# Optimization experiments

Hardware: AMD Instinct MI355X
Metric: run time of the kernel (lower is better)

Reference implementation:

```python
import jax, jax.numpy as jnp
import numpy as np

B, N, M, T, D, NH = 64, 1024, 32, 8, 512, 8
OUT = 1000
NSO, NSA = N // 4, N // 8
DH = D // NH


def _conv(x, w, b):
    y = jax.lax.conv_general_dilated(x, w, (1, 1), 'SAME', dimension_numbers=('NCHW', 'OIHW', 'NCHW'))
    return y + b[None, :, None, None]


def _bn(x, g, b):
    # BatchNorm2d in train mode: per-batch statistics over (B, H, W)
    m = x.mean(axis=(0, 2, 3), keepdims=True)
    v = x.var(axis=(0, 2, 3), keepdims=True)
    return (x - m) * jax.lax.rsqrt(v + 1e-5) * g[None, :, None, None] + b[None, :, None, None]


def _mp2(x):
    b_, c, h, w = x.shape
    return x.reshape(b_, c, h // 2, 2, w // 2, 2).max(axis=(3, 5))


def _ln(x, g, b):
    m = x.mean(-1, keepdims=True)
    v = x.var(-1, keepdims=True)
    return (x - m) * jax.lax.rsqrt(v + 1e-5) * g + b


def _glu(x):
    a, b = jnp.split(x, 2, axis=-1)
    return a * jax.nn.sigmoid(b)


def setup_inputs():
    ks = iter(jax.random.split(jax.random.key(0), 64))

    def nrm(shape, fan_in):
        return jax.random.normal(next(ks), shape, jnp.float32) / np.float32(np.sqrt(fan_in))

    inp = {}
    inp['x'] = jax.random.normal(next(ks), (B, 3, 64, 64), jnp.float32)
    inp['c1w'] = nrm((16, 3, 3, 3), 27); inp['c1b'] = jnp.zeros((16,))
    inp['bn1g'] = jnp.ones((16,)); inp['bn1b'] = jnp.zeros((16,))
    inp['c2w'] = nrm((32, 16, 3, 3), 144); inp['c2b'] = jnp.zeros((32,))
    inp['bn2g'] = jnp.ones((32,)); inp['bn2b'] = jnp.zeros((32,))
    inp['c3w'] = nrm((64, 32, 3, 3), 288); inp['c3b'] = jnp.zeros((64,))
    inp['bn3g'] = jnp.ones((64,)); inp['bn3b'] = jnp.zeros((64,))
    inp['c4w'] = nrm((64, 64, 3, 3), 576); inp['c4b'] = jnp.zeros((64,))
    inp['bn4g'] = jnp.ones((64,)); inp['bn4b'] = jnp.zeros((64,))
    inp['fc1w'] = nrm((256, 256), 256); inp['fc1b'] = jnp.zeros((256,))
    inp['fc2w'] = nrm((128, D), 128); inp['fc2b'] = jnp.zeros((D,))
    inp['kvw'] = nrm((D, D), D); inp['kvb'] = jnp.zeros((D,))
    inp['kvlg'] = jnp.ones((D,)); inp['kvlb'] = jnp.zeros((D,))
    inp['synw'] = nrm((D + N, 2 * N), D + N); inp['synb'] = jnp.zeros((2 * N,))
    inp['synlg'] = jnp.ones((N,)); inp['synlb'] = jnp.zeros((N,))
    inp['nlm_w1'] = nrm((N, M, 256), M); inp['nlm_b1'] = jnp.zeros((N, 256))
    inp['nlm_w2'] = nrm((N, 128), 128); inp['nlm_b2'] = jnp.zeros((N,))
    inp['start_act'] = nrm((N,), N)
    inp['start_trace'] = nrm((N, M), N + M)
    inp['dec_a'] = jax.random.uniform(next(ks), (NSA,), jnp.float32, 0.0, 3.0)
    inp['dec_o'] = jax.random.uniform(next(ks), (NSO,), jnp.float32, 0.0, 3.0)
    inp['qw'] = nrm((NSA, D), NSA); inp['qb'] = jnp.zeros((D,))
    inp['attn_inw'] = nrm((D, 3 * D), D); inp['attn_inb'] = jnp.zeros((3 * D,))
    inp['attn_ow'] = nrm((D, D), D); inp['attn_ob'] = jnp.zeros((D,))
    inp['op_w1'] = nrm((NSO, 256), NSO); inp['op_b1'] = jnp.zeros((256,))
    inp['op_l1g'] = jnp.ones((256,)); inp['op_l1b'] = jnp.zeros((256,))
    inp['op_w2'] = nrm((256, 64), 256); inp['op_b2'] = jnp.zeros((64,))
    inp['op_l2g'] = jnp.ones((64,)); inp['op_l2b'] = jnp.zeros((64,))
    inp['op_w3'] = nrm((64, OUT), 64); inp['op_b3'] = jnp.zeros((OUT,))
    inp['aL'] = jax.random.randint(next(ks), (NSA,), 0, N)
    inp['aR'] = jax.random.randint(next(ks), (NSA,), 0, N)
    inp['oL'] = jax.random.randint(next(ks), (NSO,), 0, N)
    inp['oR'] = jax.random.randint(next(ks), (NSO,), 0, N)
    inp['task_idx'] = 0
    return inp


def _forward(x, c1w, c1b, bn1g, bn1b, c2w, c2b, bn2g, bn2b, c3w, c3b, bn3g, bn3b, c4w, c4b, bn4g, bn4b, fc1w, fc1b, fc2w, fc2b, kvw, kvb, kvlg, kvlb, synw, synb, synlg, synlb, nlm_w1, nlm_b1, nlm_w2, nlm_b2, start_act, start_trace, dec_a, dec_o, qw, qb, attn_inw, attn_inb, attn_ow, attn_ob, op_w1, op_b1, op_l1g, op_l1b, op_w2, op_b2, op_l2g, op_l2b, op_w3, op_b3, aL, aR, oL, oR):
    # --- AdaptiveCNNEncoder (3-channel branch) ---
    h = jax.nn.relu(_bn(_conv(x, c1w, c1b), bn1g, bn1b))
    h = jax.nn.relu(_bn(_conv(h, c2w, c2b), bn2g, bn2b))
    h = _mp2(h)
    h = jax.nn.relu(_bn(_conv(h, c3w, c3b), bn3g, bn3b))
    h = _mp2(h)
    h = jax.nn.relu(_bn(_conv(h, c4w, c4b), bn4g, bn4b))
    b_, c, hh, ww = h.shape
    # AdaptiveAvgPool2d((2,2)): mean over equal blocks (16x16 -> 2x2)
    h = h.reshape(b_, c, 2, hh // 2, 2, ww // 2).mean(axis=(3, 5)).reshape(b_, c * 4)
    enc = _glu(h @ fc1w + fc1b) @ fc2w + fc2b            # (B, D)
    kv = _ln(enc @ kvw + kvb, kvlg, kvlb)                # single kv token

    Wq, Wk, Wv = jnp.split(attn_inw, 3, axis=1)
    bq, bk, bv = jnp.split(attn_inb, 3)
    kh = (kv @ Wk + bk).reshape(B, NH, DH)
    vh = (kv @ Wv + bv).reshape(B, NH, DH)

    r_a = jnp.exp(-jnp.clip(dec_a, 0.0, 15.0))           # (NSA,)
    r_o = jnp.exp(-jnp.clip(dec_o, 0.0, 15.0))           # (NSO,)

    act0 = jnp.broadcast_to(start_act, (B, N))
    trace0 = jnp.broadcast_to(start_trace, (B, N, M))
    ao0 = act0[:, oL] * act0[:, oR]                      # initial out-sync accumulators
    bo0 = jnp.ones_like(ao0)
    inv_log_out = np.float32(1.0 / np.log(OUT))
    inv_sqrt_dh = np.float32(1.0 / np.sqrt(DH))

    def tick(carry, t):
        act, trace, aa, ba, ao, bo = carry
        pp = act[:, aL] * act[:, aR]
        first = (t == 0)
        aa = jnp.where(first, pp, r_a * aa + pp)
        ba = jnp.where(first, jnp.ones_like(ba), r_a * ba + 1.0)
        sync_a = aa * jax.lax.rsqrt(ba + 1e-8)
        qv = sync_a @ qw + qb
        qh = (qv @ Wq + bq).reshape(B, NH, DH)
        logits = jnp.einsum('bhd,bhd->bh', qh, kh) * inv_sqrt_dh
        w = jax.nn.softmax(logits[..., None], axis=-1)[..., 0]  # single key -> ones
        attn_out = (w[..., None] * vh).reshape(B, D) @ attn_ow + attn_ob
        pre = jnp.concatenate([attn_out, act], axis=-1)
        state = _ln(_glu(pre @ synw + synb), synlg, synlb)
        trace = jnp.concatenate([trace[:, :, 1:], state[:, :, None]], axis=-1)
        # per-neuron private MLPs, batched: (B,N,M)x(N,M,256) -> GLU -> (N,128) -> scalar
        hid = _glu(jnp.einsum('bnm,nmh->bnh', trace, nlm_w1) + nlm_b1)
        act = jnp.einsum('bnh,nh->bn', hid, nlm_w2) + nlm_b2
        po = act[:, oL] * act[:, oR]
        ao = r_o * ao + po
        bo = r_o * bo + 1.0
        sync_o = ao * jax.lax.rsqrt(bo + 1e-8)
        h1 = jax.nn.relu(_ln(sync_o @ op_w1 + op_b1, op_l1g, op_l1b))
        h2 = jax.nn.relu(_ln(h1 @ op_w2 + op_b2, op_l2g, op_l2b))
        pred = h2 @ op_w3 + op_b3
        p = jax.nn.softmax(pred, axis=-1)
        ent = -jnp.sum(p * jnp.log(p + 1e-10), axis=-1)
        ne = ent * inv_log_out
        cert = jnp.stack([ne, 1.0 - ne], axis=-1)
        return (act, trace, aa, ba, ao, bo), (pred, cert)

    carry0 = (act0, trace0, jnp.zeros((B, NSA), jnp.float32), jnp.zeros((B, NSA), jnp.float32), ao0, bo0)
    _, (preds, certs) = jax.lax.scan(tick, carry0, jnp.arange(T))
    return jnp.transpose(preds, (1, 2, 0)), jnp.transpose(certs, (1, 2, 0))


def reference(x, c1w, c1b, bn1g, bn1b, c2w, c2b, bn2g, bn2b, c3w, c3b, bn3g, bn3b, c4w, c4b, bn4g, bn4b, fc1w, fc1b, fc2w, fc2b, kvw, kvb, kvlg, kvlb, synw, synb, synlg, synlb, nlm_w1, nlm_b1, nlm_w2, nlm_b2, start_act, start_trace, dec_a, dec_o, qw, qb, attn_inw, attn_inb, attn_ow, attn_ob, op_w1, op_b1, op_l1g, op_l1b, op_w2, op_b2, op_l2g, op_l2b, op_w3, op_b3, aL, aR, oL, oR, task_idx):
    del task_idx  # single task; all task-indexed params are for task 0
    return _forward(x, c1w, c1b, bn1g, bn1b, c2w, c2b, bn2g, bn2b, c3w, c3b, bn3g, bn3b, c4w, c4b, bn4g, bn4b, fc1w, fc1b, fc2w, fc2b, kvw, kvb, kvlg, kvlb, synw, synb, synlg, synlb, nlm_w1, nlm_b1, nlm_w2, nlm_b2, start_act, start_trace, dec_a, dec_o, qw, qb, attn_inw, attn_inb, attn_ow, attn_ob, op_w1, op_b1, op_l1g, op_l1b, op_w2, op_b2, op_l2g, op_l2b, op_w3, op_b3, aL, aR, oL, oR)
```

## Files before the change

kernel.cpp:

```cpp
#include <hip/hip_runtime.h>
#include <math.h>

constexpr int B_ = 64, N_ = 1024, M_ = 32, T_ = 8;
constexpr int OUT_ = 1000, NSO_ = 256;

#define DEVFN __device__ __forceinline__

typedef __attribute__((ext_vector_type(8))) short bf16x8;
typedef __attribute__((ext_vector_type(4))) float f32x4;

DEVFN float blockReduceSum(float v, float* buf) {
  int t = threadIdx.x;
  buf[t] = v; __syncthreads();
  for (int off = blockDim.x >> 1; off > 0; off >>= 1) {
    if (t < off) buf[t] += buf[t + off];
    __syncthreads();
  }
  float r = buf[0];
  __syncthreads();
  return r;
}

DEVFN float sigmoidf_(float x) { return 1.f / (1.f + __expf(-x)); }

DEVFN unsigned short f2bf(float f) {
  unsigned u = __float_as_uint(f);
  unsigned r = (u + 0x7FFFu + ((u >> 16) & 1u)) >> 16;
  return (unsigned short)r;
}
DEVFN float bf2f(unsigned short h) { return __uint_as_float((unsigned)h << 16); }

template<int NW>
DEVFN float bsum(float v, float* red) {
  #pragma unroll
  for (int o = 32; o > 0; o >>= 1) v += __shfl_xor(v, o);
  int w = threadIdx.x >> 6, ln = threadIdx.x & 63;
  if (ln == 0) red[w] = v;
  __syncthreads();
  if (w == 0) {
    float x = (ln < NW) ? red[ln] : 0.f;
    #pragma unroll
    for (int o = 8; o > 0; o >>= 1) x += __shfl_xor(x, o);
    if (ln == 0) red[0] = x;
  }
  __syncthreads();
  float r = red[0];
  __syncthreads();
  return r;
}

template<int NW>
DEVFN float bmax(float v, float* red) {
  #pragma unroll
  for (int o = 32; o > 0; o >>= 1) v = fmaxf(v, __shfl_xor(v, o));
  int w = threadIdx.x >> 6, ln = threadIdx.x & 63;
  if (ln == 0) red[w] = v;
  __syncthreads();
  if (w == 0) {
    float x = (ln < NW) ? red[ln] : -INFINITY;
    #pragma unroll
    for (int o = 8; o > 0; o >>= 1) x = fmaxf(x, __shfl_xor(x, o));
    if (ln == 0) red[0] = x;
  }
  __syncthreads();
  float r = red[0];
  __syncthreads();
  return r;
}

__global__ __launch_bounds__(256)
void k_w1t(const float* __restrict__ w1, unsigned short* __restrict__ w1t) {
  int n = blockIdx.x;
  __shared__ float tile[32][260];
  const float* src = w1 + (size_t)n * 8192;
  for (int i = threadIdx.x; i < 8192; i += 256)
    tile[i >> 8][i & 255] = src[i];
  __syncthreads();
  int c = threadIdx.x;
  unsigned short* dst = w1t + ((size_t)n * 256 + c) * 32;
  #pragma unroll
  for (int q = 0; q < 8; ++q) {
    ushort4 o;
    o.x = f2bf(tile[q * 4 + 0][c]); o.y = f2bf(tile[q * 4 + 1][c]);
    o.z = f2bf(tile[q * 4 + 2][c]); o.w = f2bf(tile[q * 4 + 3][c]);
    *reinterpret_cast<ushort4*>(dst + q * 4) = o;
  }
}

__global__ __launch_bounds__(256)
void k_synwt(const float* __restrict__ synw2, unsigned short* __restrict__ Bt) {
  int j0 = blockIdx.x * 64, k0 = blockIdx.y * 64;
  __shared__ float tile[64][65];
  for (int i = threadIdx.x; i < 4096; i += 256) {
    int kk = i >> 6, jj = i & 63;
    tile[kk][jj] = synw2[(size_t)(k0 + kk) * 2048 + j0 + jj];
  }
  __syncthreads();
  int jj = threadIdx.x >> 2, kq = (threadIdx.x & 3) * 16;
  unsigned short* dst = Bt + (size_t)(j0 + jj) * 1024 + k0 + kq;
  #pragma unroll
  for (int q = 0; q < 4; ++q) {
    ushort4 o;
    o.x = f2bf(tile[kq + q * 4 + 0][jj]); o.y = f2bf(tile[kq + q * 4 + 1][jj]);
    o.z = f2bf(tile[kq + q * 4 + 2][jj]); o.w = f2bf(tile[kq + q * 4 + 3][jj]);
    *reinterpret_cast<ushort4*>(dst + q * 4) = o;
  }
}

template<int CIN, int COUT, int HW, int TY, int XV, int CICH, int MODE, int KSPLIT, int COSPLIT>
__global__ __launch_bounds__(256)
void k_conv_tiled(const float* __restrict__ in, const float* __restrict__ wgl,
                  const float2* __restrict__ ssin, float* __restrict__ outp) {
  constexpr int XQ = HW / XV;
  constexpr int NCG = 4;
  constexpr int CPT = COUT / (NCG * COSPLIT);
  constexpr int PADW = HW + 8;
  constexpr int NROW = TY + 2;
  constexpr int CINB = CIN / KSPLIT;
  constexpr int NCH = CINB / CICH;
  static_assert(XQ * TY == 64, "spatial threads per co-group must be 64");
  __shared__ __align__(16) float ins[CICH][NROW][PADW];

  const int b   = blockIdx.x;
  const int y0  = blockIdx.y * TY;
  const int cs  = (COSPLIT > 1) ? (int)(blockIdx.z % COSPLIT) : 0;
  const int ks  = (KSPLIT > 1) ? (int)(blockIdx.z / COSPLIT) : 0;
  const int co0 = cs * (COUT / COSPLIT);
  const int tid = threadIdx.x;
  const int sp  = tid & 63;
  const int cg  = __builtin_amdgcn_readfirstlane(tid >> 6);
  const int xq  = sp % XQ;
  const int yr  = sp / XQ;
  const int x0  = xq * XV;

  float acc[CPT][XV];
  #pragma unroll
  for (int j = 0; j < CPT; ++j)
    #pragma unroll
    for (int k = 0; k < XV; ++k) acc[j][k] = 0.f;

  for (int ch = 0; ch < NCH; ++ch) {
    const int ci0 = ks * CINB + ch * CICH;
    __syncthreads();
    constexpr int NEL = CICH * NROW * PADW;
    for (int i = tid; i < NEL; i += 256) {
      int col = i % PADW;
      int row = (i / PADW) % NROW;
      int ci  = i / (PADW * NROW);
      int gx = col - 4;
      int gy = y0 + row - 1;
      float v = 0.f;
      if (gx >= 0 && gx < HW && gy >= 0 && gy < HW) {
        if (MODE == 0) {
          v = in[((size_t)(b * CIN + ci0 + ci) * HW + gy) * HW + gx];
        } else if (MODE == 1) {
          float2 s = ssin[ci0 + ci];
          v = fmaxf(fmaf(in[((size_t)(b * CIN + ci0 + ci) * HW + gy) * HW + gx], s.x, s.y), 0.f);
        } else {
          float2 s = ssin[ci0 + ci];
          const float* p = in + ((size_t)(b * CIN + ci0 + ci) * (2 * HW) + 2 * gy) * (2 * HW) + 2 * gx;
          float v0 = fmaf(p[0],          s.x, s.y);
          float v1 = fmaf(p[1],          s.x, s.y);
          float v2 = fmaf(p[2 * HW],     s.x, s.y);
          float v3 = fmaf(p[2 * HW + 1], s.x, s.y);
          v = fmaxf(fmaxf(fmaxf(v0, v1), fmaxf(v2, v3)), 0.f);
        }
      }
      ins[ci][row][col] = v;
    }
    __syncthreads();

    for (int ci = 0; ci < CICH; ++ci) {
      const float* wci = wgl + ((size_t)(co0 + cg * CPT) * CIN + (ci0 + ci)) * 9;
      #pragma unroll
      for (int dy = 0; dy < 3; ++dy) {
        const float* r = &ins[ci][yr + dy][x0 + 4];
        float win[XV + 2];
        win[0] = r[-1];
        if constexpr (XV == 4) {
          float4 m = *reinterpret_cast<const float4*>(r);
          win[1] = m.x; win[2] = m.y; win[3] = m.z; win[4] = m.w;
        } else if constexpr (XV == 2) {
          float2 m = *reinterpret_cast<const float2*>(r);
          win[1] = m.x; win[2] = m.y;
        } else {
          win[1] = r[0];
        }
        win[XV + 1] = r[XV];
        #pragma unroll
        for (int j = 0; j < CPT; ++j) {
          const float* wj = wci + (size_t)j * CIN * 9 + dy * 3;
          float w0 = wj[0], w1 = wj[1], w2 = wj[2];
          #pragma unroll
          for (int k = 0; k < XV; ++k)
            acc[j][k] = fmaf(win[k], w0, fmaf(win[k + 1], w1, fmaf(win[k + 2], w2, acc[j][k])));
        }
      }
    }
  }

  const size_t pofs = (size_t)ks * B_ * COUT * HW * HW;
  #pragma unroll
  for (int j = 0; j < CPT; ++j) {
    float* op = outp + pofs + (((size_t)b * COUT + co0 + cg * CPT + j) * HW + y0 + yr) * HW + x0;
    if constexpr (XV == 4)
      *reinterpret_cast<float4*>(op) = make_float4(acc[j][0], acc[j][1], acc[j][2], acc[j][3]);
    else if constexpr (XV == 2)
      *reinterpret_cast<float2*>(op) = make_float2(acc[j][0], acc[j][1]);
    else
      *op = acc[j][0];
  }
}

template<int C, int HW2, int NS>
__global__ __launch_bounds__(256)
void k_bn_stats(const float* __restrict__ x, float* __restrict__ part) {
  int c = blockIdx.x, s = blockIdx.y, ns = gridDim.y;
  const int Npc = B_ * HW2;
  constexpr size_t PSTR = (size_t)B_ * C * HW2;
  float s1 = 0.f, s2 = 0.f;
  for (int ii = s * 256 + threadIdx.x; ii < Npc; ii += ns * 256) {
    int b = ii / HW2, pos = ii % HW2;
    size_t base = ((size_t)b * C + c) * HW2 + pos;
    float v = x[base];
    #pragma unroll
    for (int q = 1; q < NS; ++q) v += x[base + q * PSTR];
    s1 += v; s2 += v * v;
  }
  __shared__ float r1[256], r2[256];
  r1[threadIdx.x] = s1; r2[threadIdx.x] = s2; __syncthreads();
  for (int off = 128; off > 0; off >>= 1) {
    if (threadIdx.x < off) { r1[threadIdx.x] += r1[threadIdx.x + off]; r2[threadIdx.x] += r2[threadIdx.x + off]; }
    __syncthreads();
  }
  if (threadIdx.x == 0) {
    part[(c * ns + s) * 2 + 0] = r1[0];
    part[(c * ns + s) * 2 + 1] = r2[0];
  }
}

__global__ void k_bn_finalize(const float* __restrict__ part, int C, int ns, float inv_n,
                              const float* __restrict__ g, const float* __restrict__ bb,
                              float2* __restrict__ ss) {
  int c = threadIdx.x;
  if (c >= C) return;
  float s1 = 0.f, s2 = 0.f;
  for (int s = 0; s < ns; ++s) { s1 += part[(c * ns + s) * 2]; s2 += part[(c * ns + s) * 2 + 1]; }
  float m = s1 * inv_n;
  float var = s2 * inv_n - m * m;
  float rstd = rsqrtf(var + 1e-5f);
  float sc = g[c] * rstd;
  ss[c] = make_float2(sc, bb[c] - m * sc);
}

__global__ __launch_bounds__(256)
void k_avgpool_bn(const float* __restrict__ x, const float2* __restrict__ ss,
                  float* __restrict__ outp) {
  constexpr size_t PSTR = (size_t)B_ * 64 * 256;
  int idx = blockIdx.x * 256 + threadIdx.x;
  if (idx >= B_ * 256) return;
  int b = idx >> 8;
  int r = idx & 255;
  int c = r >> 2, i = (r >> 1) & 1, j = r & 1;
  float2 s = ss[c];
  const float* p = x + ((size_t)(b * 64 + c) * 16 + i * 8) * 16 + j * 8;
  float sum = 0.f;
  #pragma unroll
  for (int yy = 0; yy < 8; ++yy)
    #pragma unroll
    for (int xx = 0; xx < 8; ++xx) {
      size_t o = yy * 16 + xx;
      float v = p[o] + p[o + PSTR] + p[o + 2 * PSTR] + p[o + 3 * PSTR];
      sum += fmaxf(fmaf(v, s.x, s.y), 0.f);
    }
  outp[idx] = sum * (1.f / 64.f);
}

template<int K, int NOUT>
__global__ __launch_bounds__(256)
void k_gemm_part(const float* __restrict__ A, const float* __restrict__ W, int ldw,
                 float* __restrict__ part) {
  int jt = blockIdx.x, ks = blockIdx.y;
  int k0 = ks * 64;
  __shared__ float As[64][65];
  for (int i = threadIdx.x; i < 4096; i += 256) {
    int r = i >> 6, c = i & 63;
    As[r][c] = A[(size_t)r * K + k0 + c];
  }
  __syncthreads();
  int jsub = threadIdx.x & 31;
  int bg = threadIdx.x >> 5;
  int j = jt * 32 + jsub;
  float acc[8] = {0.f, 0.f, 0.f, 0.f, 0.f, 0.f, 0.f, 0.f};
  const float* wp = W + (size_t)k0 * ldw + j;
  #pragma unroll 8
  for (int kk = 0; kk < 64; ++kk) {
    float w = wp[(size_t)kk * ldw];
    #pragma unroll
    for (int r = 0; r < 8; ++r) acc[r] = fmaf(As[bg * 8 + r][kk], w, acc[r]);
  }
  float* pp = part + (size_t)ks * 64 * NOUT + j;
  #pragma unroll
  for (int r = 0; r < 8; ++r) pp[(size_t)(bg * 8 + r) * NOUT] = acc[r];
}

__global__ __launch_bounds__(256)
void k_syn_mfma(const unsigned short* __restrict__ Abf, const unsigned short* __restrict__ Bt,
                float* __restrict__ part) {
  const int jt = blockIdx.x, ks = blockIdx.y;
  const int w = threadIdx.x >> 6, lane = threadIdx.x & 63;
  const int col = lane & 15, kg = lane >> 4;
  const int jcol = jt * 64 + w * 16 + col;
  const int k0 = ks * 256;
  f32x4 acc[4];
  #pragma unroll
  for (int mt = 0; mt < 4; ++mt) acc[mt] = (f32x4){0.f, 0.f, 0.f, 0.f};

  #pragma unroll
  for (int kb = 0; kb < 8; ++kb) {
    const int kk = k0 + kb * 32 + kg * 8;
    bf16x8 bfr = *reinterpret_cast<const bf16x8*>(Bt + (size_t)jcol * 1024 + kk);
    #pragma unroll
    for (int mt = 0; mt < 4; ++mt) {
      bf16x8 a = *reinterpret_cast<const bf16x8*>(Abf + (size_t)(mt * 16 + col) * 1024 + kk);
      acc[mt] = __builtin_amdgcn_mfma_f32_16x16x32_bf16(a, bfr, acc[mt], 0, 0, 0);
    }
  }
  #pragma unroll
  for (int mt = 0; mt < 4; ++mt) {
    int b0 = mt * 16 + kg * 4;
    #pragma unroll
    for (int r = 0; r < 4; ++r)
      part[((size_t)ks * 64 + b0 + r) * 2048 + jcol] = acc[mt][r];
  }
}

template<int NOUT, int NO_FIN, int KS, bool GLU_, bool LN_>
__global__ __launch_bounds__(256)
void k_fc_reduce(const float* __restrict__ part, const float* __restrict__ bias, int bstride,
                 const float* __restrict__ lng, const float* __restrict__ lnb,
                 float* __restrict__ outp) {
  constexpr int R = (NO_FIN + 255) / 256;
  int b = blockIdx.x, t = threadIdx.x;
  const float* bp = bias + (size_t)b * bstride;
  float v[R];
  #pragma unroll
  for (int r = 0; r < R; ++r) {
    int j = t + r * 256;
    if (j < NO_FIN) {
      float za = bp[j];
      float zb = GLU_ ? bp[j + NO_FIN] : 0.f;
      #pragma unroll
      for (int ks = 0; ks < KS; ++ks) {
        const float* pr = part + ((size_t)ks * 64 + b) * NOUT;
        za += pr[j];
        if (GLU_) zb += pr[j + NO_FIN];
      }
      v[r] = GLU_ ? za * sigmoidf_(zb) : za;
    } else v[r] = 0.f;
  }
  if (LN_) {
    __shared__ float red[256];
    float s1 = 0.f, s2 = 0.f;
    #pragma unroll
    for (int r = 0; r < R; ++r) { s1 += v[r]; s2 += v[r] * v[r]; }
    s1 = blockReduceSum(s1, red);
    s2 = blockReduceSum(s2, red);
    float mu = s1 / (float)NO_FIN;
    float rstd = rsqrtf(s2 / (float)NO_FIN - mu * mu + 1e-5f);
    #pragma unroll
    for (int r = 0; r < R; ++r) {
      int j = t + r * 256;
      if (j < NO_FIN) outp[(size_t)b * NO_FIN + j] = fmaf((v[r] - mu) * rstd, lng[j], lnb[j]);
    }
  } else {
    #pragma unroll
    for (int r = 0; r < R; ++r) {
      int j = t + r * 256;
      if (j < NO_FIN) outp[(size_t)b * NO_FIN + j] = v[r];
    }
  }
}

__global__ __launch_bounds__(1024)
void k_syn_reduce(const float* __restrict__ part, const float* __restrict__ syncst,
                  const float* __restrict__ g, const float* __restrict__ bb,
                  unsigned short* __restrict__ trace, int slot) {
  int b = blockIdx.x, t = threadIdx.x;
  __shared__ float red[16];
  float za = syncst[b * 2048 + t];
  float zb = syncst[b * 2048 + 1024 + t];
  #pragma unroll
  for (int ks = 0; ks < 4; ++ks) {
    const float* pr = part + ((size_t)ks * 64 + b) * 2048;
    za += pr[t];
    zb += pr[t + 1024];
  }
  float v = za * sigmoidf_(zb);
  float s1 = bsum<16>(v, red);
  float s2 = bsum<16>(v * v, red);
  float mu = s1 * (1.f / 1024.f);
  float rstd = rsqrtf(s2 * (1.f / 1024.f) - mu * mu + 1e-5f);
  trace[((size_t)t * 64 + b) * 32 + slot] = f2bf(fmaf((v - mu) * rstd, g[t], bb[t]));
}

__global__ __launch_bounds__(256)
void k_init(const float* __restrict__ sa, const float* __restrict__ st,
            const int* __restrict__ oL, const int* __restrict__ oR,
            float* __restrict__ act, unsigned short* __restrict__ act_bf,
            unsigned short* __restrict__ trace,
            float* __restrict__ ao, float* __restrict__ bo) {
  int idx = blockIdx.x * 256 + threadIdx.x;
  if (idx < B_ * N_ * M_) {
    int n = idx >> 11, m = idx & 31;
    trace[idx] = f2bf(st[n * 32 + m]);
  }
  if (idx < B_ * N_) {
    float v = sa[idx % N_];
    act[idx] = v;
    act_bf[idx] = f2bf(v);
  }
  if (idx < B_ * NSO_) {
    int i = idx % NSO_;
    ao[idx] = sa[oL[i]] * sa[oR[i]];
    bo[idx] = 1.f;
  }
}

__global__ __launch_bounds__(128)
void k_nlm_mfma(const unsigned short* __restrict__ trace, const unsigned short* __restrict__ w1t,
                const float* __restrict__ b1, const float* __restrict__ w2,
                const float* __restrict__ b2, float* __restrict__ act,
                unsigned short* __restrict__ act_bf, int tick) {
  const int w = threadIdx.x >> 6, lane = threadIdx.x & 63;
  const int n = blockIdx.x * 2 + w;
  const int col = lane & 15, kg = lane >> 4;
  __shared__ __align__(16) unsigned short ldsA[2][64][40];
  {
    const uint4* src = reinterpret_cast<const uint4*>(trace + ((size_t)n * 64 + lane) * 32);
    uint4 r0 = src[0], r1 = src[1], r2 = src[2], r3 = src[3];
    uint4* d = reinterpret_cast<uint4*>(&ldsA[w][lane][0]);
    d[0] = r0; d[1] = r1; d[2] = r2; d[3] = r3;
  }
  bf16x8 bf[16];
  float b1v[16], w2v[8];
  #pragma unroll
  for (int nt = 0; nt < 16; ++nt) {
    bf[nt] = *reinterpret_cast<const bf16x8*>(w1t + (((size_t)n * 256 + nt * 16 + col) * 32 + kg * 8));
    b1v[nt] = b1[n * 256 + nt * 16 + col];
  }
  #pragma unroll
  for (int nt = 0; nt < 8; ++nt) w2v[nt] = w2[n * 128 + nt * 16 + col];
  const float b2n = b2[n];
  const int kbase = kg * 8 + ((tick + 1) & 31);
  __syncthreads();
  #pragma unroll
  for (int mt = 0; mt < 4; ++mt) {
    const int brow = mt * 16 + col;
    bf16x8 af;
    #pragma unroll
    for (int j = 0; j < 8; ++j)
      af[j] = (short)ldsA[w][brow][(kbase + j) & 31];
    f32x4 acc[16];
    #pragma unroll
    for (int nt = 0; nt < 16; ++nt)
      acc[nt] = __builtin_amdgcn_mfma_f32_16x16x32_bf16(af, bf[nt], (f32x4){0.f, 0.f, 0.f, 0.f}, 0, 0, 0);
    float v0 = 0.f, v1 = 0.f, v2 = 0.f, v3 = 0.f;
    #pragma unroll
    for (int nt = 0; nt < 8; ++nt) {
      f32x4 za = acc[nt], zb = acc[nt + 8];
      float ba = b1v[nt], bg = b1v[nt + 8], wv = w2v[nt];
      v0 = fmaf((za[0] + ba) * sigmoidf_(zb[0] + bg), wv, v0);
      v1 = fmaf((za[1] + ba) * sigmoidf_(zb[1] + bg), wv, v1);
      v2 = fmaf((za[2] + ba) * sigmoidf_(zb[2] + bg), wv, v2);
      v3 = fmaf((za[3] + ba) * sigmoidf_(zb[3] + bg), wv, v3);
    }
    #pragma unroll
    for (int o = 1; o <= 8; o <<= 1) {
      v0 += __shfl_xor(v0, o); v1 += __shfl_xor(v1, o);
      v2 += __shfl_xor(v2, o); v3 += __shfl_xor(v3, o);
    }
    if (col == 0) {
      int b0 = mt * 16 + kg * 4;
      float r0 = v0 + b2n, r1 = v1 + b2n, r2 = v2 + b2n, r3 = v3 + b2n;
      act[(size_t)(b0 + 0) * 1024 + n] = r0;
      act[(size_t)(b0 + 1) * 1024 + n] = r1;
      act[(size_t)(b0 + 2) * 1024 + n] = r2;
      act[(size_t)(b0 + 3) * 1024 + n] = r3;
      act_bf[(size_t)(b0 + 0) * 1024 + n] = f2bf(r0);
      act_bf[(size_t)(b0 + 1) * 1024 + n] = f2bf(r1);
      act_bf[(size_t)(b0 + 2) * 1024 + n] = f2bf(r2);
      act_bf[(size_t)(b0 + 3) * 1024 + n] = f2bf(r3);
    }
  }
}

__global__ __launch_bounds__(1024)
void k_outpath(const float* __restrict__ act, float* __restrict__ ao, float* __restrict__ bo,
               const float* __restrict__ dec_o, const int* __restrict__ oL, const int* __restrict__ oR,
               const float* __restrict__ opw1, const float* __restrict__ opb1,
               const float* __restrict__ l1g, const float* __restrict__ l1b,
               const float* __restrict__ opw2, const float* __restrict__ opb2,
               const float* __restrict__ l2g, const float* __restrict__ l2b,
               const float* __restrict__ opw3, const float* __restrict__ opb3,
               float* __restrict__ outp, int tick) {
  int b = blockIdx.x, t = threadIdx.x;
  __shared__ float red[16];
  __shared__ float syo[256], h1s[256], h2s[64];
  __shared__ float zp1[4][256];
  __shared__ float zp2[16][64];
  const float* actb = act + (size_t)b * 1024;
  if (t < 256) {
    float po = actb[oL[t]] * actb[oR[t]];
    float r = __expf(-fminf(fmaxf(dec_o[t], 0.f), 15.f));
    int ai = b * 256 + t;
    float av = fmaf(r, ao[ai], po);
    float bv = fmaf(r, bo[ai], 1.f);
    ao[ai] = av; bo[ai] = bv;
    syo[t] = av * rsqrtf(bv + 1e-8f);
  }
  __syncthreads();
  {
    int j = t & 255, ks = t >> 8;
    float z = 0.f;
    const float* wcol = opw1 + j;
    #pragma unroll 8
    for (int k = ks * 64; k < ks * 64 + 64; ++k) z = fmaf(syo[k], wcol[k * 256], z);
    zp1[ks][j] = z;
  }
  __syncthreads();
  float h1v = 0.f;
  if (t < 256) h1v = zp1[0][t] + zp1[1][t] + zp1[2][t] + zp1[3][t] + opb1[t];
  float s1 = bsum<16>(t < 256 ? h1v : 0.f, red);
  float s2 = bsum<16>(t < 256 ? h1v * h1v : 0.f, red);
  if (t < 256) {
    float mu = s1 * (1.f / 256.f);
    float rstd = rsqrtf(s2 * (1.f / 256.f) - mu * mu + 1e-5f);
    h1s[t] = fmaxf(fmaf((h1v - mu) * rstd, l1g[t], l1b[t]), 0.f);
  }
  __syncthreads();
  {
    int j = t & 63, ks = t >> 6;
    float z = 0.f;
    const float* wcol = opw2 + j;
    #pragma unroll
    for (int k = ks * 16; k < ks * 16 + 16; ++k) z = fmaf(h1s[k], wcol[k * 64], z);
    zp2[ks][j] = z;
  }
  __syncthreads();
  if (t < 64) {
    float z2 = opb2[t];
    #pragma unroll
    for (int ks = 0; ks < 16; ++ks) z2 += zp2[ks][t];
    float a1 = z2, a2 = z2 * z2;
    #pragma unroll
    for (int o = 32; o > 0; o >>= 1) { a1 += __shfl_xor(a1, o); a2 += __shfl_xor(a2, o); }
    float mu2 = a1 * (1.f / 64.f);
    float rs2 = rsqrtf(a2 * (1.f / 64.f) - mu2 * mu2 + 1e-5f);
    h2s[t] = fmaxf(fmaf((z2 - mu2) * rs2, l2g[t], l2b[t]), 0.f);
  }
  __syncthreads();
  float z3 = 0.f;
  if (t < OUT_) {
    z3 = opb3[t];
    const float* wcol = opw3 + t;
    #pragma unroll 8
    for (int k = 0; k < 64; ++k) z3 = fmaf(h2s[k], wcol[k * OUT_], z3);
    outp[(size_t)b * (OUT_ * T_) + (size_t)t * T_ + tick] = z3;
  }
  float mx = bmax<16>(t < OUT_ ? z3 : -INFINITY, red);
  float e = (t < OUT_) ? __expf(z3 - mx) : 0.f;
  float S = bsum<16>(e, red);
  float inv = 1.f / S;
  float ep = 0.f;
  if (t < OUT_) {
    float p = e * inv;
    ep = p * __logf(p + 1e-10f);
  }
  float ent = -bsum<16>(ep, red);
  if (t == 0) {
    float ne = ent * (1.f / logf(1000.f));
    outp[(size_t)B_ * OUT_ * T_ + (size_t)b * 2 * T_ + tick]      = ne;
    outp[(size_t)B_ * OUT_ * T_ + (size_t)b * 2 * T_ + T_ + tick] = 1.f - ne;
  }
}

extern "C" void kernel_launch(void* const* d_in, const int* in_sizes, int n_in,
                              void* d_out, int out_size, void* d_ws, size_t ws_size,
                              hipStream_t stream) {
  (void)in_sizes; (void)n_in; (void)out_size; (void)ws_size;
  const float* x      = (const float*)d_in[0];
  const float* c1w    = (const float*)d_in[1];
  const float* bn1g   = (const float*)d_in[3];
  const float* bn1b   = (const float*)d_in[4];
  const float* c2w    = (const float*)d_in[5];
  const float* bn2g   = (const float*)d_in[7];
  const float* bn2b   = (const float*)d_in[8];
  const float* c3w    = (const float*)d_in[9];
  const float* bn3g   = (const float*)d_in[11];
  const float* bn3b   = (const float*)d_in[12];
  const float* c4w    = (const float*)d_in[13];
  const float* bn4g   = (const float*)d_in[15];
  const float* bn4b   = (const float*)d_in[16];
  const float* fc1w   = (const float*)d_in[17];
  const float* fc1b   = (const float*)d_in[18];
  const float* fc2w   = (const float*)d_in[19];
  const float* fc2b   = (const float*)d_in[20];
  const float* kvw    = (const float*)d_in[21];
  const float* kvb    = (const float*)d_in[22];
  const float* kvlg   = (const float*)d_in[23];
  const float* kvlb   = (const float*)d_in[24];
  const float* synw   = (const float*)d_in[25];
  const float* synb   = (const float*)d_in[26];
  const float* synlg  = (const float*)d_in[27];
  const float* synlb  = (const float*)d_in[28];
  const float* nlmw1  = (const float*)d_in[29];
  const float* nlmb1  = (const float*)d_in[30];
  const float* nlmw2  = (const float*)d_in[31];
  const float* nlmb2  = (const float*)d_in[32];
  const float* sact   = (const float*)d_in[33];
  const float* strc   = (const float*)d_in[34];
  const float* dec_o  = (const float*)d_in[36];
  const float* attn_inw = (const float*)d_in[39];
  const float* attn_inb = (const float*)d_in[40];
  const float* attn_ow  = (const float*)d_in[41];
  const float* attn_ob  = (const float*)d_in[42];
  const float* opw1   = (const float*)d_in[43];
  const float* opb1   = (const float*)d_in[44];
  const float* opl1g  = (const float*)d_in[45];
  const float* opl1b  = (const float*)d_in[46];
  const float* opw2   = (const float*)d_in[47];
  const float* opb2   = (const float*)d_in[48];
  const float* opl2g  = (const float*)d_in[49];
  const float* opl2b  = (const float*)d_in[50];
  const float* opw3   = (const float*)d_in[51];
  const float* opb3   = (const float*)d_in[52];
  const int*   oL     = (const int*)d_in[55];
  const int*   oR     = (const int*)d_in[56];
  float* outp = (float*)d_out;
  float* ws   = (float*)d_ws;

  float* c2raw = ws;
  float* c4part= ws;
  float* c1raw = ws + 8388608;
  float* c3raw = ws + 8388608;
  float* part  = ws + 4194304;
  unsigned short* trace_bf = (unsigned short*)(ws + 6291456);
  float* act   = ws + 8388608;
  float* syncst= ws + 8454144;
  float* pooled= ws + 8585216;
  float* ench  = ws + 8601600;
  float* enc   = ws + 8609792;
  float* kvbuf = ws + 8642560;
  float* vhbuf = ws + 8675328;
  float* aout  = ws + 8708096;
  float* ao    = ws + 8740864;
  float* bo    = ws + 8757248;
  unsigned short* w1t_bf   = (unsigned short*)(ws + 8777728);
  unsigned short* synw2t_bf= (unsigned short*)(ws + 12972032);
  float* bnpart= ws + 14020608;
  float2* bnss = (float2*)(ws + 14024704);
  unsigned short* act_bf = (unsigned short*)(ws + 14028800);

  k_conv_tiled<3,16,64,4,4,3,0,1,1><<<dim3(64,16),256,0,stream>>>(x, c1w, nullptr, c1raw);
  k_bn_stats<16,4096,1><<<dim3(16,32),256,0,stream>>>(c1raw, bnpart);
  k_bn_finalize<<<1,64,0,stream>>>(bnpart, 16, 32, 1.f/(float)(B_*4096), bn1g, bn1b, bnss);

  k_conv_tiled<16,32,64,2,2,16,1,1,1><<<dim3(64,32),256,0,stream>>>(c1raw, c2w, bnss, c2raw);
  k_bn_stats<32,4096,1><<<dim3(32,32),256,0,stream>>>(c2raw, bnpart);
  k_bn_finalize<<<1,64,0,stream>>>(bnpart, 32, 32, 1.f/(float)(B_*4096), bn2g, bn2b, bnss);

  k_conv_tiled<32,64,32,4,2,16,2,1,2><<<dim3(64,8,2),256,0,stream>>>(c2raw, c3w, bnss, c3raw);
  k_bn_stats<64,1024,1><<<dim3(64,16),256,0,stream>>>(c3raw, bnpart);
  k_bn_finalize<<<1,64,0,stream>>>(bnpart, 64, 16, 1.f/(float)(B_*1024), bn3g, bn3b, bnss);

  k_conv_tiled<64,64,16,4,1,16,2,4,1><<<dim3(64,4,4),256,0,stream>>>(c3raw, c4w, bnss, c4part);

  k_w1t<<<1024,256,0,stream>>>(nlmw1, w1t_bf);
  k_synwt<<<dim3(32,16),256,0,stream>>>(synw + (size_t)512 * 2048, synw2t_bf);

  k_bn_stats<64,256,4><<<dim3(64,8),256,0,stream>>>(c4part, bnpart);
  k_bn_finalize<<<1,64,0,stream>>>(bnpart, 64, 8, 1.f/(float)(B_*256), bn4g, bn4b, bnss);
  k_avgpool_bn<<<64,256,0,stream>>>(c4part, bnss, pooled);

  k_gemm_part<256,256><<<dim3(8,4),256,0,stream>>>(pooled, fc1w, 256, part);
  k_fc_reduce<256,128,4,true,false><<<64,256,0,stream>>>(part, fc1b, 0, nullptr, nullptr, ench);
  k_gemm_part<128,512><<<dim3(16,2),256,0,stream>>>(ench, fc2w, 512, part);
  k_fc_reduce<512,512,2,false,false><<<64,256,0,stream>>>(part, fc2b, 0, nullptr, nullptr, enc);
  k_gemm_part<512,512><<<dim3(16,8),256,0,stream>>>(enc, kvw, 512, part);
  k_fc_reduce<512,512,8,false,true><<<64,256,0,stream>>>(part, kvb, 0, kvlg, kvlb, kvbuf);
  k_gemm_part<512,512><<<dim3(16,8),256,0,stream>>>(kvbuf, attn_inw + 1024, 1536, part);
  k_fc_reduce<512,512,8,false,false><<<64,256,0,stream>>>(part, attn_inb + 1024, 0, nullptr, nullptr, vhbuf);
  k_gemm_part<512,512><<<dim3(16,8),256,0,stream>>>(vhbuf, attn_ow, 512, part);
  k_fc_reduce<512,512,8,false,false><<<64,256,0,stream>>>(part, attn_ob, 0, nullptr, nullptr, aout);
  k_gemm_part<512,2048><<<dim3(64,8),256,0,stream>>>(aout, synw, 2048, part);
  k_fc_reduce<2048,2048,8,false,false><<<64,256,0,stream>>>(part, synb, 0, nullptr, nullptr, syncst);

  k_init<<<8192,256,0,stream>>>(sact, strc, oL, oR, act, act_bf, trace_bf, ao, bo);

  for (int t = 0; t < T_; ++t) {
    k_syn_mfma<<<dim3(32,4),256,0,stream>>>(act_bf, synw2t_bf, part);
    k_syn_reduce<<<64,1024,0,stream>>>(part, syncst, synlg, synlb, trace_bf, t);
    k_nlm_mfma<<<512,128,0,stream>>>(trace_bf, w1t_bf, nlmb1, nlmw2, nlmb2, act, act_bf, t);
    k_outpath<<<64,1024,0,stream>>>(act, ao, bo, dec_o, oL, oR,
                                    opw1, opb1, opl1g, opl1b,
                                    opw2, opb2, opl2g, opl2b,
                                    opw3, opb3, outp, t);
  }
}
```

Before: 595.2 us.

## Store conv intermediates as bf16 and fold BN finalize into consumer kernels

Conv1–3 outputs are now written as bf16 instead of fp32, and the following BN-stats and conv kernels read them as bf16. This halves the bytes moved for the large activation tensors. The separate BN finalize launches are removed: each consumer conv block, and the avgpool kernel, recomputes the per-channel scale and shift from the partial sums into shared memory. In exchange, intermediates lose precision, and every block repeats a small reduction over the partials.

```diff
diff --git a/kernel.cpp b/kernel.cpp
--- a/kernel.cpp
+++ b/kernel.cpp
@@ -107,10 +107,13 @@
   }
 }
 
-template<int CIN, int COUT, int HW, int TY, int XV, int CICH, int MODE, int KSPLIT, int COSPLIT>
-__global__ __launch_bounds__(256)
-void k_conv_tiled(const float* __restrict__ in, const float* __restrict__ wgl,
-                  const float2* __restrict__ ssin, float* __restrict__ outp) {
+template<int CIN, int COUT, int HW, int TY, int XV, int CICH, int MODE, int KSPLIT, int COSPLIT,
+         bool INBF, bool OUTBF>
+__global__ __launch_bounds__(256)
+void k_conv_tiled(const void* __restrict__ in_, const float* __restrict__ wgl,
+                  const float* __restrict__ bnpart, const float* __restrict__ bng,
+                  const float* __restrict__ bnb, int ns, float inv_n,
+                  void* __restrict__ outp_) {
   constexpr int XQ = HW / XV;
   constexpr int NCG = 4;
   constexpr int CPT = COUT / (NCG * COSPLIT);
@@ -120,6 +123,10 @@
   constexpr int NCH = CINB / CICH;
   static_assert(XQ * TY == 64, "spatial threads per co-group must be 64");
   __shared__ __align__(16) float ins[CICH][NROW][PADW];
+  __shared__ float2 ssl[(MODE != 0) ? CIN : 1];
+
+  const float* inf = (const float*)in_;
+  const unsigned short* inb = (const unsigned short*)in_;
 
   const int b   = blockIdx.x;
   const int y0  = blockIdx.y * TY;
@@ -132,6 +139,19 @@
   const int xq  = sp % XQ;
   const int yr  = sp / XQ;
   const int x0  = xq * XV;
+
+  if (MODE != 0) {
+    for (int c = tid; c < CIN; c += 256) {
+      float s1 = 0.f, s2 = 0.f;
+      for (int s = 0; s < ns; ++s) { s1 += bnpart[(c * ns + s) * 2]; s2 += bnpart[(c * ns + s) * 2 + 1]; }
+      float m = s1 * inv_n;
+      float var = s2 * inv_n - m * m;
+      float rstd = rsqrtf(var + 1e-5f);
+      float sc = bng[c] * rstd;
+      ssl[c] = make_float2(sc, bnb[c] - m * sc);
+    }
+    __syncthreads();
+  }
 
   float acc[CPT][XV];
   #pragma unroll
@@ -152,17 +172,25 @@
       float v = 0.f;
       if (gx >= 0 && gx < HW && gy >= 0 && gy < HW) {
         if (MODE == 0) {
-          v = in[((size_t)(b * CIN + ci0 + ci) * HW + gy) * HW + gx];
+          v = inf[((size_t)(b * CIN + ci0 + ci) * HW + gy) * HW + gx];
         } else if (MODE == 1) {
-          float2 s = ssin[ci0 + ci];
-          v = fmaxf(fmaf(in[((size_t)(b * CIN + ci0 + ci) * HW + gy) * HW + gx], s.x, s.y), 0.f);
+          float2 s = ssl[ci0 + ci];
+          size_t idx = ((size_t)(b * CIN + ci0 + ci) * HW + gy) * HW + gx;
+          float raw = INBF ? bf2f(inb[idx]) : inf[idx];
+          v = fmaxf(fmaf(raw, s.x, s.y), 0.f);
         } else {
-          float2 s = ssin[ci0 + ci];
-          const float* p = in + ((size_t)(b * CIN + ci0 + ci) * (2 * HW) + 2 * gy) * (2 * HW) + 2 * gx;
-          float v0 = fmaf(p[0],          s.x, s.y);
-          float v1 = fmaf(p[1],          s.x, s.y);
-          float v2 = fmaf(p[2 * HW],     s.x, s.y);
-          float v3 = fmaf(p[2 * HW + 1], s.x, s.y);
+          float2 s = ssl[ci0 + ci];
+          size_t base = ((size_t)(b * CIN + ci0 + ci) * (2 * HW) + 2 * gy) * (2 * HW) + 2 * gx;
+          float r0, r1, r2, r3;
+          if (INBF) {
+            r0 = bf2f(inb[base]);            r1 = bf2f(inb[base + 1]);
+            r2 = bf2f(inb[base + 2 * HW]);   r3 = bf2f(inb[base + 2 * HW + 1]);
+          } else {
+            r0 = inf[base];            r1 = inf[base + 1];
+            r2 = inf[base + 2 * HW];   r3 = inf[base + 2 * HW + 1];
+          }
+          float v0 = fmaf(r0, s.x, s.y), v1 = fmaf(r1, s.x, s.y);
+          float v2 = fmaf(r2, s.x, s.y), v3 = fmaf(r3, s.x, s.y);
           v = fmaxf(fmaxf(fmaxf(v0, v1), fmaxf(v2, v3)), 0.f);
         }
       }
@@ -202,13 +230,53 @@
   const size_t pofs = (size_t)ks * B_ * COUT * HW * HW;
   #pragma unroll
   for (int j = 0; j < CPT; ++j) {
-    float* op = outp + pofs + (((size_t)b * COUT + co0 + cg * CPT + j) * HW + y0 + yr) * HW + x0;
-    if constexpr (XV == 4)
-      *reinterpret_cast<float4*>(op) = make_float4(acc[j][0], acc[j][1], acc[j][2], acc[j][3]);
-    else if constexpr (XV == 2)
-      *reinterpret_cast<float2*>(op) = make_float2(acc[j][0], acc[j][1]);
-    else
-      *op = acc[j][0];
+    size_t oidx = pofs + (((size_t)b * COUT + co0 + cg * CPT + j) * HW + y0 + yr) * HW + x0;
+    if constexpr (OUTBF) {
+      unsigned short* op = (unsigned short*)outp_ + oidx;
+      if constexpr (XV == 4) {
+        ushort4 o; o.x = f2bf(acc[j][0]); o.y = f2bf(acc[j][1]); o.z = f2bf(acc[j][2]); o.w = f2bf(acc[j][3]);
+        *reinterpret_cast<ushort4*>(op) = o;
+      } else if constexpr (XV == 2) {
+        ushort2 o; o.x = f2bf(acc[j][0]); o.y = f2bf(acc[j][1]);
+        *reinterpret_cast<ushort2*>(op) = o;
+      } else {
+        *op = f2bf(acc[j][0]);
+      }
+    } else {
+      float* op = (float*)outp_ + oidx;
+      if constexpr (XV == 4)
+        *reinterpret_cast<float4*>(op) = make_float4(acc[j][0], acc[j][1], acc[j][2], acc[j][3]);
+      else if constexpr (XV == 2)
+        *reinterpret_cast<float2*>(op) = make_float2(acc[j][0], acc[j][1]);
+      else
+        *op = acc[j][0];
+    }
+  }
+}
+
+template<int C, int HW2>
+__global__ __launch_bounds__(256)
+void k_bn_stats_bf(const unsigned short* __restrict__ x, float* __restrict__ part) {
+  int c = blockIdx.x, s = blockIdx.y, ns = gridDim.y;
+  const int Np2 = B_ * HW2 / 2;
+  float s1 = 0.f, s2 = 0.f;
+  for (int ii = s * 256 + threadIdx.x; ii < Np2; ii += ns * 256) {
+    int b = ii / (HW2 / 2), p2 = ii % (HW2 / 2);
+    const unsigned short* pp = x + ((size_t)b * C + c) * HW2 + p2 * 2;
+    unsigned u = *reinterpret_cast<const unsigned*>(pp);
+    float v0 = __uint_as_float(u << 16);
+    float v1 = __uint_as_float(u & 0xFFFF0000u);
+    s1 += v0 + v1; s2 += v0 * v0 + v1 * v1;
+  }
+  __shared__ float r1[256], r2[256];
+  r1[threadIdx.x] = s1; r2[threadIdx.x] = s2; __syncthreads();
+  for (int off = 128; off > 0; off >>= 1) {
+    if (threadIdx.x < off) { r1[threadIdx.x] += r1[threadIdx.x + off]; r2[threadIdx.x] += r2[threadIdx.x + off]; }
+    __syncthreads();
+  }
+  if (threadIdx.x == 0) {
+    part[(c * ns + s) * 2 + 0] = r1[0];
+    part[(c * ns + s) * 2 + 1] = r2[0];
   }
 }
 
@@ -239,30 +307,30 @@
   }
 }
 
-__global__ void k_bn_finalize(const float* __restrict__ part, int C, int ns, float inv_n,
-                              const float* __restrict__ g, const float* __restrict__ bb,
-                              float2* __restrict__ ss) {
-  int c = threadIdx.x;
-  if (c >= C) return;
-  float s1 = 0.f, s2 = 0.f;
-  for (int s = 0; s < ns; ++s) { s1 += part[(c * ns + s) * 2]; s2 += part[(c * ns + s) * 2 + 1]; }
-  float m = s1 * inv_n;
-  float var = s2 * inv_n - m * m;
-  float rstd = rsqrtf(var + 1e-5f);
-  float sc = g[c] * rstd;
-  ss[c] = make_float2(sc, bb[c] - m * sc);
-}
-
-__global__ __launch_bounds__(256)
-void k_avgpool_bn(const float* __restrict__ x, const float2* __restrict__ ss,
+__global__ __launch_bounds__(256)
+void k_avgpool_bn(const float* __restrict__ x, const float* __restrict__ bnpart,
+                  const float* __restrict__ g, const float* __restrict__ bb,
                   float* __restrict__ outp) {
   constexpr size_t PSTR = (size_t)B_ * 64 * 256;
-  int idx = blockIdx.x * 256 + threadIdx.x;
-  if (idx >= B_ * 256) return;
+  constexpr int NSns = 8;
+  __shared__ float2 ssl[64];
+  int t = threadIdx.x;
+  if (t < 64) {
+    float s1 = 0.f, s2 = 0.f;
+    for (int s = 0; s < NSns; ++s) { s1 += bnpart[(t * NSns + s) * 2]; s2 += bnpart[(t * NSns + s) * 2 + 1]; }
+    float inv_n = 1.f / (float)(B_ * 256);
+    float m = s1 * inv_n;
+    float var = s2 * inv_n - m * m;
+    float rstd = rsqrtf(var + 1e-5f);
+    float sc = g[t] * rstd;
+    ssl[t] = make_float2(sc, bb[t] - m * sc);
+  }
+  __syncthreads();
+  int idx = blockIdx.x * 256 + t;
   int b = idx >> 8;
   int r = idx & 255;
   int c = r >> 2, i = (r >> 1) & 1, j = r & 1;
-  float2 s = ss[c];
+  float2 s = ssl[c];
   const float* p = x + ((size_t)(b * 64 + c) * 16 + i * 8) * 16 + j * 8;
   float sum = 0.f;
   #pragma unroll
@@ -640,10 +708,10 @@
   float* outp = (float*)d_out;
   float* ws   = (float*)d_ws;
 
-  float* c2raw = ws;
+  unsigned short* c1raw_bf = (unsigned short*)(ws + 8388608);
+  unsigned short* c2raw_bf = (unsigned short*)ws;
+  unsigned short* c3raw_bf = (unsigned short*)(ws + 8388608);
   float* c4part= ws;
-  float* c1raw = ws + 8388608;
-  float* c3raw = ws + 8388608;
   float* part  = ws + 4194304;
   unsigned short* trace_bf = (unsigned short*)(ws + 6291456);
   float* act   = ws + 8388608;
@@ -659,29 +727,32 @@
   unsigned short* w1t_bf   = (unsigned short*)(ws + 8777728);
   unsigned short* synw2t_bf= (unsigned short*)(ws + 12972032);
   float* bnpart= ws + 14020608;
-  float2* bnss = (float2*)(ws + 14024704);
   unsigned short* act_bf = (unsigned short*)(ws + 14028800);
 
-  k_conv_tiled<3,16,64,4,4,3,0,1,1><<<dim3(64,16),256,0,stream>>>(x, c1w, nullptr, c1raw);
-  k_bn_stats<16,4096,1><<<dim3(16,32),256,0,stream>>>(c1raw, bnpart);
-  k_bn_finalize<<<1,64,0,stream>>>(bnpart, 16, 32, 1.f/(float)(B_*4096), bn1g, bn1b, bnss);
-
-  k_conv_tiled<16,32,64,2,2,16,1,1,1><<<dim3(64,32),256,0,stream>>>(c1raw, c2w, bnss, c2raw);
-  k_bn_stats<32,4096,1><<<dim3(32,32),256,0,stream>>>(c2raw, bnpart);
-  k_bn_finalize<<<1,64,0,stream>>>(bnpart, 32, 32, 1.f/(float)(B_*4096), bn2g, bn2b, bnss);
-
-  k_conv_tiled<32,64,32,4,2,16,2,1,2><<<dim3(64,8,2),256,0,stream>>>(c2raw, c3w, bnss, c3raw);
-  k_bn_stats<64,1024,1><<<dim3(64,16),256,0,stream>>>(c3raw, bnpart);
-  k_bn_finalize<<<1,64,0,stream>>>(bnpart, 64, 16, 1.f/(float)(B_*1024), bn3g, bn3b, bnss);
-
-  k_conv_tiled<64,64,16,4,1,16,2,4,1><<<dim3(64,4,4),256,0,stream>>>(c3raw, c4w, bnss, c4part);
+  const float inv1 = 1.f / (float)(B_ * 4096);
+  const float inv2 = 1.f / (float)(B_ * 4096);
+  const float inv3 = 1.f / (float)(B_ * 1024);
+
+  k_conv_tiled<3,16,64,4,4,3,0,1,1,false,true><<<dim3(64,16),256,0,stream>>>(
+      x, c1w, nullptr, nullptr, nullptr, 0, 0.f, c1raw_bf);
+  k_bn_stats_bf<16,4096><<<dim3(16,32),256,0,stream>>>(c1raw_bf, bnpart);
+
+  k_conv_tiled<16,32,64,2,2,16,1,1,1,true,true><<<dim3(64,32),256,0,stream>>>(
+      c1raw_bf, c2w, bnpart, bn1g, bn1b, 32, inv1, c2raw_bf);
+  k_bn_stats_bf<32,4096><<<dim3(32,32),256,0,stream>>>(c2raw_bf, bnpart);
+
+  k_conv_tiled<32,64,32,4,2,16,2,1,2,true,true><<<dim3(64,8,2),256,0,stream>>>(
+      c2raw_bf, c3w, bnpart, bn2g, bn2b, 32, inv2, c3raw_bf);
+  k_bn_stats_bf<64,1024><<<dim3(64,16),256,0,stream>>>(c3raw_bf, bnpart);
+
+  k_conv_tiled<64,64,16,4,1,16,2,4,1,true,false><<<dim3(64,4,4),256,0,stream>>>(
+      c3raw_bf, c4w, bnpart, bn3g, bn3b, 16, inv3, c4part);
 
   k_w1t<<<1024,256,0,stream>>>(nlmw1, w1t_bf);
   k_synwt<<<dim3(32,16),256,0,stream>>>(synw + (size_t)512 * 2048, synw2t_bf);
 
   k_bn_stats<64,256,4><<<dim3(64,8),256,0,stream>>>(c4part, bnpart);
-  k_bn_finalize<<<1,64,0,stream>>>(bnpart, 64, 8, 1.f/(float)(B_*256), bn4g, bn4b, bnss);
-  k_avgpool_bn<<<64,256,0,stream>>>(c4part, bnss, pooled);
+  k_avgpool_bn<<<64,256,0,stream>>>(c4part, bnpart, bn4g, bn4b, pooled);
 
   k_gemm_part<256,256><<<dim3(8,4),256,0,stream>>>(pooled, fc1w, 256, part);
   k_fc_reduce<256,128,4,true,false><<<64,256,0,stream>>>(part, fc1b, 0, nullptr, nullptr, ench);
```

New measurement: 575.5 us. -3.3%, faster.
